# Kernel optimization log

Measured on AMD Instinct MI355X. Metric: run time of the kernel, lower is better.

## Reference

```python
import jax, jax.numpy as jnp
import numpy as np

C = 256
HEADS = 8
HD = C // HEADS
SCALE = HD ** -0.5


def conv1x1(x, W, b):
    # x: [B,C_in,H,W], W: [C_out,C_in], b: [C_out]
    return jnp.einsum('oc,bchw->bohw', W, x) + b[None, :, None, None]


def setup_inputs() -> dict:
    key = jax.random.key(0)
    ks = jax.random.split(key, 12)
    B, H, Wd = 2, 48, 48
    s = C ** -0.5
    return {
        'x': jax.random.normal(ks[0], (B, C, H, Wd), jnp.float32),
        'uncertainty': jax.random.uniform(ks[1], (B, 1, H, Wd), jnp.float32),
        'Wq': jax.random.normal(ks[2], (C, C), jnp.float32) * s,
        'bq': jnp.zeros((C,), jnp.float32),
        'Wk': jax.random.normal(ks[3], (C, C), jnp.float32) * s,
        'bk': jnp.zeros((C,), jnp.float32),
        'Wv': jax.random.normal(ks[4], (C, C), jnp.float32) * s,
        'bv': jnp.zeros((C,), jnp.float32),
        'Wg': jax.random.normal(ks[5], (C, 1), jnp.float32),
        'bg': jnp.zeros((C,), jnp.float32),
        'Wo': jax.random.normal(ks[6], (C, C), jnp.float32) * s,
        'bo': jnp.zeros((C,), jnp.float32),
    }


def reference(x, uncertainty, Wq, bq, Wk, bk, Wv, bv, Wg, bg, Wo, bo):
    B, _, H, Wd = x.shape
    N = H * Wd
    # uncertainty gate (1x1 conv from 1 channel to C channels)
    uw = conv1x1(uncertainty, Wg, bg)            # [B,C,H,W]
    gated_x = x * (1.0 - uw)
    q = conv1x1(gated_x, Wq, bq).reshape(B, HEADS, HD, N)
    k = conv1x1(gated_x, Wk, bk).reshape(B, HEADS, HD, N)
    v = conv1x1(x, Wv, bv).reshape(B, HEADS, HD, N)
    # scores: [B,h,N,N] (query tokens n, key tokens m)
    scores = jnp.einsum('bhdn,bhdm->bhnm', q, k) * SCALE
    u_flat = uncertainty.reshape(B, 1, 1, N)      # mask over key axis
    scores = scores * (1.0 - u_flat)
    attn = jax.nn.softmax(scores, axis=-1)
    out = jnp.einsum('bhnm,bhdm->bhdn', attn, v)  # [B,h,hd,N]
    out = out.reshape(B, C, H, Wd)
    out = conv1x1(out, Wo, bo)
    return out + x
```

## Files before the change

### kernel.cpp

```cpp
#include <hip/hip_runtime.h>
#include <hip/hip_bf16.h>

typedef float f32x4 __attribute__((ext_vector_type(4)));
typedef __bf16 bf16x8 __attribute__((ext_vector_type(8)));
typedef __bf16 bf16x4 __attribute__((ext_vector_type(4)));
typedef short s16x4 __attribute__((ext_vector_type(4)));

constexpr int C = 256;
constexpr int N = 2304;
constexpr int T = 2 * N;

#if __has_builtin(__builtin_amdgcn_exp2f)
#define EXP2F(x) __builtin_amdgcn_exp2f(x)
#else
#define EXP2F(x) exp2f(x)
#endif

__device__ __forceinline__ bf16x8 load_bf8(const __bf16* p) {
    return *reinterpret_cast<const bf16x8*>(p);
}

__device__ __forceinline__ f32x4 mfma32(bf16x8 a, bf16x8 b, f32x4 c) {
    return __builtin_amdgcn_mfma_f32_16x16x32_bf16(a, b, c, 0, 0, 0);
}

#if __has_builtin(__builtin_amdgcn_mfma_f32_16x16x16bf16_1k)
__device__ __forceinline__ f32x4 mfma16(bf16x4 a, bf16x4 b, f32x4 c) {
    return __builtin_amdgcn_mfma_f32_16x16x16bf16_1k(
        __builtin_bit_cast(s16x4, a), __builtin_bit_cast(s16x4, b), c, 0, 0, 0);
}
#else
__device__ __forceinline__ f32x4 mfma16(bf16x4 a, bf16x4 b, f32x4 c) {
    f32x4 d;
    asm volatile("v_mfma_f32_16x16x16_bf16 %0, %1, %2, %3"
                 : "=v"(d) : "v"(a), "v"(b), "v"(c));
    return d;
}
#endif

__device__ __forceinline__ void gload_lds16(const __bf16* g, __bf16* l) {
    __builtin_amdgcn_global_load_lds(
        (const __attribute__((address_space(1))) void*)g,
        (__attribute__((address_space(3))) void*)l, 16, 0, 0);
}

#define VMCNT0() asm volatile("s_waitcnt vmcnt(0)" ::: "memory")
#define LGKM0()  asm volatile("s_waitcnt lgkmcnt(0)" ::: "memory")

__global__ void wconv_kernel(const float* __restrict__ Wq, const float* __restrict__ Wk,
                             const float* __restrict__ Wv, const float* __restrict__ Wo,
                             __bf16* __restrict__ Wb) {
    const float* srcs[4] = {Wq, Wk, Wv, Wo};
    int m = blockIdx.x >> 6;
    int idx = (blockIdx.x & 63) * 256 + threadIdx.x;
    float4 v = reinterpret_cast<const float4*>(srcs[m])[idx];
    bf16x4 o = { (__bf16)v.x, (__bf16)v.y, (__bf16)v.z, (__bf16)v.w };
    reinterpret_cast<bf16x4*>(Wb + m * 65536)[idx] = o;
}

__global__ void prep_kernel(const float* __restrict__ x, const float* __restrict__ u,
                            const float* __restrict__ Wg, const float* __restrict__ bg,
                            __bf16* __restrict__ xT, __bf16* __restrict__ gxT) {
    __shared__ float tile[32][65];
    int b = blockIdx.z, c0 = blockIdx.y * 32, n0 = blockIdx.x * 64;
    int t = threadIdx.x;
    const float* xp = x + (b * C + c0) * N + n0;
    #pragma unroll
    for (int r = 0; r < 8; ++r) {
        int cl = r * 4 + (t >> 6);
        int nl = t & 63;
        tile[cl][nl] = xp[cl * N + nl];
    }
    __syncthreads();
    int cq = (t & 7) * 4;
    #pragma unroll
    for (int it = 0; it < 2; ++it) {
        int nl = it * 32 + (t >> 3);
        float uv = u[b * N + n0 + nl];
        bf16x4 xo, go;
        #pragma unroll
        for (int j = 0; j < 4; ++j) {
            int c = c0 + cq + j;
            float xv = tile[cq + j][nl];
            float gate = 1.0f - (Wg[c] * uv + bg[c]);
            xo[j] = (__bf16)xv;
            go[j] = (__bf16)(xv * gate);
        }
        int tok = b * N + n0 + nl;
        *reinterpret_cast<bf16x4*>(xT + (long)tok * C + c0 + cq) = xo;
        *reinterpret_cast<bf16x4*>(gxT + (long)tok * C + c0 + cq) = go;
    }
}

__global__ __launch_bounds__(256) void qkv_kernel(const __bf16* __restrict__ Wb,
    const __bf16* __restrict__ xT, const __bf16* __restrict__ gxT,
    const float* __restrict__ bq, const float* __restrict__ bk, const float* __restrict__ bv,
    const float* __restrict__ u,
    __bf16* __restrict__ Q, __bf16* __restrict__ K, __bf16* __restrict__ V) {
    int proj = blockIdx.z;
    int o0 = blockIdx.y * 64;
    int t0 = blockIdx.x * 32;
    int wave = threadIdx.x >> 6, lane = threadIdx.x & 63;
    int g = lane >> 4, r = lane & 15;
    int ow = o0 + wave * 16;
    const __bf16* W = Wb + proj * 65536;
    const __bf16* inp = (proj == 2) ? xT : gxT;
    f32x4 acc[2] = {};
    for (int k = 0; k < 8; ++k) {
        bf16x8 a = load_bf8(W + (ow + r) * C + k * 32 + g * 8);
        #pragma unroll
        for (int tb = 0; tb < 2; ++tb) {
            bf16x8 bfr = load_bf8(inp + (long)(t0 + tb * 16 + r) * C + k * 32 + g * 8);
            acc[tb] = mfma32(a, bfr, acc[tb]);
        }
    }
    const float* bias = (proj == 0) ? bq : (proj == 1) ? bk : bv;
    float bvw[4];
    #pragma unroll
    for (int i = 0; i < 4; ++i) bvw[i] = bias[ow + g * 4 + i];
    int h = ow >> 5, d0 = (ow & 31) + g * 4;
    const float SC = 0.17677669529663687f * 1.4426950408889634f;
    #pragma unroll
    for (int tb = 0; tb < 2; ++tb) {
        int t = t0 + tb * 16 + r;
        int b = t / N, n = t % N;
        if (proj == 2) {
            #pragma unroll
            for (int i = 0; i < 4; ++i)
                V[((long)(b * 8 + h) * 32 + d0 + i) * N + n] = (__bf16)(acc[tb][i] + bvw[i]);
        } else {
            bf16x4 outv;
            if (proj == 1) {
                float scale = SC * (1.0f - u[t]);
                #pragma unroll
                for (int i = 0; i < 4; ++i) outv[i] = (__bf16)((acc[tb][i] + bvw[i]) * scale);
            } else {
                #pragma unroll
                for (int i = 0; i < 4; ++i) outv[i] = (__bf16)(acc[tb][i] + bvw[i]);
            }
            __bf16* dst = (proj == 0) ? Q : K;
            *reinterpret_cast<bf16x4*>(dst + ((long)(b * 8 + h) * N + n) * 32 + d0) = outv;
        }
    }
}

__global__ __launch_bounds__(256) void attn_kernel(const __bf16* __restrict__ Q,
    const __bf16* __restrict__ K, const __bf16* __restrict__ V,
    __bf16* __restrict__ aoT) {
    __shared__ __bf16 sMem[8192];
    __bf16* sK = sMem;
    __bf16* sV = sMem + 4096;
    int id = blockIdx.x;
    int xcd = id & 7, j = id >> 3;
    int bh = xcd + 8 * (j / 72);
    int qblk = j % 72;
    int tid = threadIdx.x;
    int wave = tid >> 6, lane = tid & 63;
    int wp = wave & 1, pair = wave >> 1;
    int g = lane >> 4, r = lane & 15;
    int q0 = qblk * 32;
    const __bf16* Qg = Q + (long)bh * N * 32;
    const __bf16* Kg = K + (long)bh * N * 32 + (long)pair * 1152 * 32;
    const __bf16* Vg = V + (long)bh * 32 * N + pair * 1152;
    bf16x8 qf = load_bf8(Qg + (q0 + wp * 16 + r) * 32 + g * 8);
    int s_ = wp * 64 + lane;
    int l_ = s_ ^ ((s_ >> 3) & 7);
    const __bf16* kSrc = Kg + (l_ >> 2) * 32 + (l_ & 3) * 8;
    const __bf16* vSrc = Vg + (long)(l_ >> 2) * N + (l_ & 3) * 8;
    __bf16* kd0 = sK + pair * 2048;
    __bf16* vd0 = sV + pair * 2048;
    auto STAGE = [&](long m0, int buf) {
        gload_lds16(kSrc + m0 * 32, kd0 + buf * 1024 + wp * 512);
        gload_lds16(vSrc + m0,      vd0 + buf * 1024 + wp * 512);
    };
    int key = (r >> 1) & 7;
    int pk0 = ((r * 4 + g) ^ key) * 8;
    int pk1 = (((16 + r) * 4 + g) ^ key) * 8;
    int pv00 = (((r) * 4 + 0 + (g >> 1)) ^ key) * 8 + (g & 1) * 4;
    int pv01 = (((16 + r) * 4 + 0 + (g >> 1)) ^ key) * 8 + (g & 1) * 4;
    int pv10 = (((r) * 4 + 2 + (g >> 1)) ^ key) * 8 + (g & 1) * 4;
    int pv11 = (((16 + r) * 4 + 2 + (g >> 1)) ^ key) * 8 + (g & 1) * 4;
    bf16x4 onesv;
    #pragma unroll
    for (int i = 0; i < 4; ++i) onesv[i] = (__bf16)1.0f;
    f32x4 oa0 = {}, oa1 = {}, oal = {};
    STAGE(0, 0);
    for (int t = 0; t < 36; ++t) {
        LGKM0();
        VMCNT0();
        __builtin_amdgcn_s_barrier();
        const __bf16* kb = kd0 + (t & 1) * 1024;
        const __bf16* vb = vd0 + (t & 1) * 1024;
        if (t < 35) STAGE((long)(t + 1) * 32, (t & 1) ^ 1);
        bf16x8 kc0 = load_bf8(kb + pk0);
        bf16x8 kc1 = load_bf8(kb + pk1);
        bf16x4 vf00 = *reinterpret_cast<const bf16x4*>(vb + pv00);
        bf16x4 vf01 = *reinterpret_cast<const bf16x4*>(vb + pv01);
        bf16x4 vf10 = *reinterpret_cast<const bf16x4*>(vb + pv10);
        bf16x4 vf11 = *reinterpret_cast<const bf16x4*>(vb + pv11);
        f32x4 z = {};
        __builtin_amdgcn_s_setprio(1);
        f32x4 s0 = mfma32(kc0, qf, z);
        f32x4 s1 = mfma32(kc1, qf, z);
        __builtin_amdgcn_s_setprio(0);
        bf16x4 pa0, pa1;
        #pragma unroll
        for (int i = 0; i < 4; ++i) pa0[i] = (__bf16)EXP2F(s0[i]);
        #pragma unroll
        for (int i = 0; i < 4; ++i) pa1[i] = (__bf16)EXP2F(s1[i]);
        __builtin_amdgcn_s_setprio(1);
        oa0 = mfma16(vf00, pa0, oa0);
        oa1 = mfma16(vf01, pa0, oa1);
        oal = mfma16(onesv, pa0, oal);
        oa0 = mfma16(vf10, pa1, oa0);
        oa1 = mfma16(vf11, pa1, oa1);
        oal = mfma16(onesv, pa1, oal);
        __builtin_amdgcn_s_setprio(0);
    }
    __builtin_amdgcn_s_barrier();
    float* F = reinterpret_cast<float*>(sMem);
    *reinterpret_cast<f32x4*>(F + wave * 512 + r * 32 + g * 4) = oa0;
    *reinterpret_cast<f32x4*>(F + wave * 512 + r * 32 + 16 + g * 4) = oa1;
    if (g == 0) F[2048 + wave * 16 + r] = oal[0];
    __builtin_amdgcn_s_barrier();
    if (tid < 128) {
        int q = tid >> 2;
        int wpq = q >> 4, qq = q & 15;
        int d8 = (tid & 3) * 8;
        int base0 = wpq * 512 + qq * 32 + d8;
        int base1 = (wpq + 2) * 512 + qq * 32 + d8;
        f32x4 a0 = *reinterpret_cast<f32x4*>(F + base0) +
                   *reinterpret_cast<f32x4*>(F + base1);
        f32x4 a1 = *reinterpret_cast<f32x4*>(F + base0 + 4) +
                   *reinterpret_cast<f32x4*>(F + base1 + 4);
        float l = F[2048 + wpq * 16 + qq] + F[2048 + (wpq + 2) * 16 + qq];
        float inv = 1.0f / l;
        bf16x8 ov;
        #pragma unroll
        for (int i = 0; i < 4; ++i) {
            ov[i] = (__bf16)(a0[i] * inv);
            ov[4 + i] = (__bf16)(a1[i] * inv);
        }
        int b = bh >> 3, h = bh & 7;
        *reinterpret_cast<bf16x8*>(aoT + (long)(b * N + q0 + q) * C + h * 32 + d8) = ov;
    }
}

__global__ __launch_bounds__(256) void outp_kernel(const __bf16* __restrict__ Wb,
    const __bf16* __restrict__ aoT, const float* __restrict__ bo,
    const float* __restrict__ x, float* __restrict__ out) {
    int o0 = blockIdx.y * 64;
    int t0 = blockIdx.x * 16;
    int wave = threadIdx.x >> 6, lane = threadIdx.x & 63;
    int g = lane >> 4, r = lane & 15;
    int ow = o0 + wave * 16;
    const __bf16* W = Wb + 3 * 65536;
    f32x4 acc = {};
    for (int k = 0; k < 8; ++k) {
        bf16x8 a = load_bf8(W + (ow + r) * C + k * 32 + g * 8);
        bf16x8 bfr = load_bf8(aoT + (long)(t0 + r) * C + k * 32 + g * 8);
        acc = mfma32(a, bfr, acc);
    }
    float bvw[4];
    #pragma unroll
    for (int i = 0; i < 4; ++i) bvw[i] = bo[ow + g * 4 + i];
    int t = t0 + r;
    int b = t / N, n = t % N;
    #pragma unroll
    for (int i = 0; i < 4; ++i) {
        long idx = ((long)b * C + ow + g * 4 + i) * N + n;
        out[idx] = acc[i] + bvw[i] + x[idx];
    }
}

extern "C" void kernel_launch(void* const* d_in, const int* in_sizes, int n_in,
                              void* d_out, int out_size, void* d_ws, size_t ws_size,
                              hipStream_t stream) {
    const float* x  = (const float*)d_in[0];
    const float* u  = (const float*)d_in[1];
    const float* Wq = (const float*)d_in[2];
    const float* bq = (const float*)d_in[3];
    const float* Wk = (const float*)d_in[4];
    const float* bk = (const float*)d_in[5];
    const float* Wv = (const float*)d_in[6];
    const float* bv = (const float*)d_in[7];
    const float* Wg = (const float*)d_in[8];
    const float* bg = (const float*)d_in[9];
    const float* Wo = (const float*)d_in[10];
    const float* bo = (const float*)d_in[11];
    float* out = (float*)d_out;

    char* ws = (char*)d_ws;
    size_t off = 0;
    auto alloc = [&](size_t bytes) {
        char* p = ws + off;
        off += (bytes + 255) & ~(size_t)255;
        return p;
    };
    __bf16* Wb  = (__bf16*)alloc((size_t)4 * 65536 * 2);
    __bf16* xT  = (__bf16*)alloc((size_t)T * C * 2);
    __bf16* gxT = (__bf16*)alloc((size_t)T * C * 2);
    __bf16* Qb  = (__bf16*)alloc((size_t)16 * N * 32 * 2);
    __bf16* Kb  = (__bf16*)alloc((size_t)16 * N * 32 * 2);
    __bf16* Vb  = (__bf16*)alloc((size_t)16 * N * 32 * 2);
    __bf16* aoT = (__bf16*)alloc((size_t)T * C * 2);

    wconv_kernel<<<256, 256, 0, stream>>>(Wq, Wk, Wv, Wo, Wb);
    prep_kernel<<<dim3(36, 8, 2), 256, 0, stream>>>(x, u, Wg, bg, xT, gxT);
    qkv_kernel<<<dim3(144, 4, 3), 256, 0, stream>>>(Wb, xT, gxT, bq, bk, bv, u, Qb, Kb, Vb);
    attn_kernel<<<1152, 256, 0, stream>>>(Qb, Kb, Vb, aoT);
    outp_kernel<<<dim3(288, 4), 256, 0, stream>>>(Wb, aoT, bo, x, out);
}
```

Baseline: 78.26 us.

## Give each attention wave a private key range and both query tiles

Each of the four waves now owns a quarter of the key sequence and handles all 32 queries, so every wave stages its own K/V tiles into a private LDS region. This drops the per-iteration block barrier and LDS wait, and lets each K/V fragment load feed twice as many MFMAs. The final reduction now sums four partial accumulators instead of two. LDS use doubles and register pressure rises from the extra accumulators, and each wave now runs an 18-step loop with a shorter pipeline.

```diff
diff --git a/kernel.cpp b/kernel.cpp
--- a/kernel.cpp
+++ b/kernel.cpp
@@ -45,7 +45,6 @@
 }
 
 #define VMCNT0() asm volatile("s_waitcnt vmcnt(0)" ::: "memory")
-#define LGKM0()  asm volatile("s_waitcnt lgkmcnt(0)" ::: "memory")
 
 __global__ void wconv_kernel(const float* __restrict__ Wq, const float* __restrict__ Wk,
                              const float* __restrict__ Wv, const float* __restrict__ Wo,
@@ -147,51 +146,49 @@
 __global__ __launch_bounds__(256) void attn_kernel(const __bf16* __restrict__ Q,
     const __bf16* __restrict__ K, const __bf16* __restrict__ V,
     __bf16* __restrict__ aoT) {
-    __shared__ __bf16 sMem[8192];
-    __bf16* sK = sMem;
-    __bf16* sV = sMem + 4096;
+    __shared__ __bf16 sMem[16384];
     int id = blockIdx.x;
     int xcd = id & 7, j = id >> 3;
     int bh = xcd + 8 * (j / 72);
     int qblk = j % 72;
     int tid = threadIdx.x;
     int wave = tid >> 6, lane = tid & 63;
-    int wp = wave & 1, pair = wave >> 1;
     int g = lane >> 4, r = lane & 15;
     int q0 = qblk * 32;
     const __bf16* Qg = Q + (long)bh * N * 32;
-    const __bf16* Kg = K + (long)bh * N * 32 + (long)pair * 1152 * 32;
-    const __bf16* Vg = V + (long)bh * 32 * N + pair * 1152;
-    bf16x8 qf = load_bf8(Qg + (q0 + wp * 16 + r) * 32 + g * 8);
-    int s_ = wp * 64 + lane;
-    int l_ = s_ ^ ((s_ >> 3) & 7);
-    const __bf16* kSrc = Kg + (l_ >> 2) * 32 + (l_ & 3) * 8;
-    const __bf16* vSrc = Vg + (long)(l_ >> 2) * N + (l_ & 3) * 8;
-    __bf16* kd0 = sK + pair * 2048;
-    __bf16* vd0 = sV + pair * 2048;
+    const __bf16* Kg = K + (long)bh * N * 32 + (long)wave * 576 * 32;
+    const __bf16* Vg = V + (long)bh * 32 * N + wave * 576;
+    bf16x8 qf0 = load_bf8(Qg + (q0 + r) * 32 + g * 8);
+    bf16x8 qf1 = load_bf8(Qg + (q0 + 16 + r) * 32 + g * 8);
+    int l0 = lane ^ ((lane >> 3) & 7);
+    const __bf16* kS = Kg + (l0 >> 2) * 32 + (l0 & 3) * 8;
+    const __bf16* vS = Vg + (long)(l0 >> 2) * N + (l0 & 3) * 8;
+    __bf16* kB = sMem + wave * 4096;
+    __bf16* vB = kB + 2048;
     auto STAGE = [&](long m0, int buf) {
-        gload_lds16(kSrc + m0 * 32, kd0 + buf * 1024 + wp * 512);
-        gload_lds16(vSrc + m0,      vd0 + buf * 1024 + wp * 512);
+        gload_lds16(kS + m0 * 32,       kB + buf * 1024);
+        gload_lds16(kS + m0 * 32 + 512, kB + buf * 1024 + 512);
+        gload_lds16(vS + m0,            vB + buf * 1024);
+        gload_lds16(vS + 16 * N + m0,   vB + buf * 1024 + 512);
     };
     int key = (r >> 1) & 7;
     int pk0 = ((r * 4 + g) ^ key) * 8;
     int pk1 = (((16 + r) * 4 + g) ^ key) * 8;
-    int pv00 = (((r) * 4 + 0 + (g >> 1)) ^ key) * 8 + (g & 1) * 4;
+    int pv00 = ((r * 4 + 0 + (g >> 1)) ^ key) * 8 + (g & 1) * 4;
     int pv01 = (((16 + r) * 4 + 0 + (g >> 1)) ^ key) * 8 + (g & 1) * 4;
-    int pv10 = (((r) * 4 + 2 + (g >> 1)) ^ key) * 8 + (g & 1) * 4;
+    int pv10 = ((r * 4 + 2 + (g >> 1)) ^ key) * 8 + (g & 1) * 4;
     int pv11 = (((16 + r) * 4 + 2 + (g >> 1)) ^ key) * 8 + (g & 1) * 4;
     bf16x4 onesv;
     #pragma unroll
     for (int i = 0; i < 4; ++i) onesv[i] = (__bf16)1.0f;
-    f32x4 oa0 = {}, oa1 = {}, oal = {};
+    f32x4 oa00 = {}, oa01 = {}, oa10 = {}, oa11 = {};
+    f32x4 oal0 = {}, oal1 = {};
     STAGE(0, 0);
-    for (int t = 0; t < 36; ++t) {
-        LGKM0();
+    for (int t = 0; t < 18; ++t) {
         VMCNT0();
-        __builtin_amdgcn_s_barrier();
-        const __bf16* kb = kd0 + (t & 1) * 1024;
-        const __bf16* vb = vd0 + (t & 1) * 1024;
-        if (t < 35) STAGE((long)(t + 1) * 32, (t & 1) ^ 1);
+        const __bf16* kb = kB + (t & 1) * 1024;
+        const __bf16* vb = vB + (t & 1) * 1024;
+        if (t < 17) STAGE((long)(t + 1) * 32, (t & 1) ^ 1);
         bf16x8 kc0 = load_bf8(kb + pk0);
         bf16x8 kc1 = load_bf8(kb + pk1);
         bf16x4 vf00 = *reinterpret_cast<const bf16x4*>(vb + pv00);
@@ -200,49 +197,64 @@
         bf16x4 vf11 = *reinterpret_cast<const bf16x4*>(vb + pv11);
         f32x4 z = {};
         __builtin_amdgcn_s_setprio(1);
-        f32x4 s0 = mfma32(kc0, qf, z);
-        f32x4 s1 = mfma32(kc1, qf, z);
+        f32x4 s00 = mfma32(kc0, qf0, z);
+        f32x4 s01 = mfma32(kc1, qf0, z);
+        f32x4 s10 = mfma32(kc0, qf1, z);
+        f32x4 s11 = mfma32(kc1, qf1, z);
         __builtin_amdgcn_s_setprio(0);
-        bf16x4 pa0, pa1;
-        #pragma unroll
-        for (int i = 0; i < 4; ++i) pa0[i] = (__bf16)EXP2F(s0[i]);
-        #pragma unroll
-        for (int i = 0; i < 4; ++i) pa1[i] = (__bf16)EXP2F(s1[i]);
+        bf16x4 pa00, pa01, pa10, pa11;
+        #pragma unroll
+        for (int i = 0; i < 4; ++i) pa00[i] = (__bf16)EXP2F(s00[i]);
+        #pragma unroll
+        for (int i = 0; i < 4; ++i) pa01[i] = (__bf16)EXP2F(s01[i]);
+        #pragma unroll
+        for (int i = 0; i < 4; ++i) pa10[i] = (__bf16)EXP2F(s10[i]);
+        #pragma unroll
+        for (int i = 0; i < 4; ++i) pa11[i] = (__bf16)EXP2F(s11[i]);
         __builtin_amdgcn_s_setprio(1);
-        oa0 = mfma16(vf00, pa0, oa0);
-        oa1 = mfma16(vf01, pa0, oa1);
-        oal = mfma16(onesv, pa0, oal);
-        oa0 = mfma16(vf10, pa1, oa0);
-        oa1 = mfma16(vf11, pa1, oa1);
-        oal = mfma16(onesv, pa1, oal);
+        oa00 = mfma16(vf00, pa00, oa00);
+        oa01 = mfma16(vf01, pa00, oa01);
+        oal0 = mfma16(onesv, pa00, oal0);
+        oa00 = mfma16(vf10, pa01, oa00);
+        oa01 = mfma16(vf11, pa01, oa01);
+        oal0 = mfma16(onesv, pa01, oal0);
+        oa10 = mfma16(vf00, pa10, oa10);
+        oa11 = mfma16(vf01, pa10, oa11);
+        oal1 = mfma16(onesv, pa10, oal1);
+        oa10 = mfma16(vf10, pa11, oa10);
+        oa11 = mfma16(vf11, pa11, oa11);
+        oal1 = mfma16(onesv, pa11, oal1);
         __builtin_amdgcn_s_setprio(0);
     }
-    __builtin_amdgcn_s_barrier();
+    __syncthreads();
     float* F = reinterpret_cast<float*>(sMem);
-    *reinterpret_cast<f32x4*>(F + wave * 512 + r * 32 + g * 4) = oa0;
-    *reinterpret_cast<f32x4*>(F + wave * 512 + r * 32 + 16 + g * 4) = oa1;
-    if (g == 0) F[2048 + wave * 16 + r] = oal[0];
-    __builtin_amdgcn_s_barrier();
-    if (tid < 128) {
-        int q = tid >> 2;
-        int wpq = q >> 4, qq = q & 15;
-        int d8 = (tid & 3) * 8;
-        int base0 = wpq * 512 + qq * 32 + d8;
-        int base1 = (wpq + 2) * 512 + qq * 32 + d8;
-        f32x4 a0 = *reinterpret_cast<f32x4*>(F + base0) +
-                   *reinterpret_cast<f32x4*>(F + base1);
-        f32x4 a1 = *reinterpret_cast<f32x4*>(F + base0 + 4) +
-                   *reinterpret_cast<f32x4*>(F + base1 + 4);
-        float l = F[2048 + wpq * 16 + qq] + F[2048 + (wpq + 2) * 16 + qq];
+    float* D = F + 4096;
+    *reinterpret_cast<f32x4*>(F + wave * 1024 + r * 32 + g * 4) = oa00;
+    *reinterpret_cast<f32x4*>(F + wave * 1024 + r * 32 + 16 + g * 4) = oa01;
+    *reinterpret_cast<f32x4*>(F + wave * 1024 + 512 + r * 32 + g * 4) = oa10;
+    *reinterpret_cast<f32x4*>(F + wave * 1024 + 512 + r * 32 + 16 + g * 4) = oa11;
+    if (g == 0) {
+        D[wave * 32 + r] = oal0[0];
+        D[wave * 32 + 16 + r] = oal1[0];
+    }
+    __syncthreads();
+    {
+        int q = tid >> 3;
+        int d4 = (tid & 7) * 4;
+        int qt = q >> 4, qq = q & 15;
+        int base = qt * 512 + qq * 32 + d4;
+        f32x4 sum = *reinterpret_cast<f32x4*>(F + base) +
+                    *reinterpret_cast<f32x4*>(F + 1024 + base) +
+                    *reinterpret_cast<f32x4*>(F + 2048 + base) +
+                    *reinterpret_cast<f32x4*>(F + 3072 + base);
+        float l = D[qt * 16 + qq] + D[32 + qt * 16 + qq] +
+                  D[64 + qt * 16 + qq] + D[96 + qt * 16 + qq];
         float inv = 1.0f / l;
-        bf16x8 ov;
-        #pragma unroll
-        for (int i = 0; i < 4; ++i) {
-            ov[i] = (__bf16)(a0[i] * inv);
-            ov[4 + i] = (__bf16)(a1[i] * inv);
-        }
+        bf16x4 ov;
+        #pragma unroll
+        for (int i = 0; i < 4; ++i) ov[i] = (__bf16)(sum[i] * inv);
         int b = bh >> 3, h = bh & 7;
-        *reinterpret_cast<bf16x8*>(aoT + (long)(b * N + q0 + q) * C + h * 32 + d8) = ov;
+        *reinterpret_cast<bf16x4*>(aoT + (long)(b * N + q0 + q) * C + h * 32 + d4) = ov;
     }
 }
 
```

Measured after the change: 77.73 us. No clear change (-0.7%).
